# Kernel tuning notes

Hardware: AMD Instinct MI355X
Metric: run time of the kernel (lower is better)

Reference implementation:

```python
import jax, jax.numpy as jnp
import numpy as np

POOL_H, POOL_W = 7, 7
SCALE = 0.25
SAMPLING = 2  # fixed sampling ratio (static grid)


def _sample_coords(lo, bin_sz, pool, s):
    # lo: [N], bin_sz: [N] -> coords [N, pool*s]
    # point iy within bin: (iy + 0.5) / s of a bin
    offs = (jnp.arange(pool)[:, None] + (jnp.arange(s)[None, :] + 0.5) / s).reshape(-1)  # [pool*s]
    return lo[:, None] + offs[None, :] * bin_sz[:, None]


def roi_align(feat, rois, roibatches):
    B, C, H, W = feat.shape
    N = rois.shape[0]
    x1 = rois[:, 0] * SCALE
    y1 = rois[:, 1] * SCALE
    x2 = rois[:, 2] * SCALE
    y2 = rois[:, 3] * SCALE
    roi_w = jnp.maximum(x2 - x1, 1.0)
    roi_h = jnp.maximum(y2 - y1, 1.0)
    bin_w = roi_w / POOL_W
    bin_h = roi_h / POOL_H

    ys = _sample_coords(y1, bin_h, POOL_H, SAMPLING)  # [N, Gy]
    xs = _sample_coords(x1, bin_w, POOL_W, SAMPLING)  # [N, Gx]
    Gy, Gx = ys.shape[1], xs.shape[1]

    vy = (ys >= -1.0) & (ys <= H)  # out-of-range samples contribute 0
    vx = (xs >= -1.0) & (xs <= W)

    yc = jnp.clip(ys, 0.0, H - 1)
    xc = jnp.clip(xs, 0.0, W - 1)
    y_lo = jnp.clip(jnp.floor(yc).astype(jnp.int32), 0, H - 1)
    x_lo = jnp.clip(jnp.floor(xc).astype(jnp.int32), 0, W - 1)
    y_hi = jnp.minimum(y_lo + 1, H - 1)
    x_hi = jnp.minimum(x_lo + 1, W - 1)
    ly = yc - y_lo  # [N, Gy]
    lx = xc - x_lo  # [N, Gx]
    hy = 1.0 - ly
    hx = 1.0 - lx

    b = roibatches.astype(jnp.int32)[:, None, None]  # [N,1,1]

    def gather(yi, xi):
        # advanced indexing -> [N, Gy, Gx, C]
        return feat[b, :, yi[:, :, None], xi[:, None, :]]

    v_ll = gather(y_lo, x_lo)
    v_lh = gather(y_lo, x_hi)
    v_hl = gather(y_hi, x_lo)
    v_hh = gather(y_hi, x_hi)

    wy_l = (hy * vy)[:, :, None, None]
    wy_h = (ly * vy)[:, :, None, None]
    wx_l = (hx * vx)[:, None, :, None]
    wx_h = (lx * vx)[:, None, :, None]

    vals = (wy_l * wx_l * v_ll + wy_l * wx_h * v_lh
            + wy_h * wx_l * v_hl + wy_h * wx_h * v_hh)  # [N, Gy, Gx, C]

    # average pool over the SAMPLING x SAMPLING points per bin
    vals = vals.reshape(N, POOL_H, SAMPLING, POOL_W, SAMPLING, C)
    out = vals.mean(axis=(2, 4))  # [N, POOL_H, POOL_W, C]
    return jnp.transpose(out, (0, 3, 1, 2))  # [N, C, POOL_H, POOL_W]


def setup_inputs() -> dict:
    key = jax.random.key(0)
    k1, k2, k3, k4 = jax.random.split(key, 4)
    B, C, H, W = 4, 256, 200, 304
    N = 1024
    img_h, img_w = H / SCALE, W / SCALE
    feat = jax.random.normal(k1, (B, C, H, W), dtype=jnp.float32)
    xa = jax.random.uniform(k2, (N, 2), minval=0.0, maxval=img_w)
    ya = jax.random.uniform(k3, (N, 2), minval=0.0, maxval=img_h)
    rois = jnp.stack([xa.min(1), ya.min(1), xa.max(1), ya.max(1)], axis=1).astype(jnp.float32)
    roibatches = jax.random.randint(k4, (N,), 0, B, dtype=jnp.int32)
    return {"feat": feat, "rois": rois, "roibatches": roibatches}


def reference(feat, rois, roibatches):
    return roi_align(feat, rois, roibatches)
```

## Files before the change

kernel.cpp:

```cpp
#include <hip/hip_runtime.h>
#include <hip/hip_bf16.h>


#define POOL 7
constexpr int Bc = 4;
constexpr int Cc = 256;
constexpr int Hc = 200;
constexpr int Wc = 304;
constexpr int HWc = Hc * Wc;
constexpr float SCALEc = 0.25f;

static __device__ __forceinline__ float bf16_lo(unsigned u) {
    u <<= 16;
    return __builtin_bit_cast(float, u);
}
static __device__ __forceinline__ float bf16_hi(unsigned u) {
    u &= 0xFFFF0000u;
    return __builtin_bit_cast(float, u);
}
static __device__ __forceinline__ unsigned pack_bf16(float f0, float f1) {
    unsigned u0 = (unsigned)__hip_bfloat16_raw(__float2bfloat16(f0)).x;
    unsigned u1 = (unsigned)__hip_bfloat16_raw(__float2bfloat16(f1)).x;
    return u0 | (u1 << 16);
}

__global__ __launch_bounds__(256) void nchw_to_nhwc_bf16(
    const float* __restrict__ in, ushort* __restrict__ outp)
{
    __shared__ float tile[128][65];
    int b  = blockIdx.z;
    int p0 = blockIdx.x * 64;
    int c0 = blockIdx.y * 128;
    int tx = threadIdx.x;
    int ty = threadIdx.y;

    const float* src = in + ((size_t)b * Cc + c0) * (size_t)HWc + p0;
#pragma unroll
    for (int k = 0; k < 32; ++k) {
        int c = ty + 4 * k;
        tile[c][tx ^ ((c >> 5) & 3)] = src[(size_t)c * HWc + tx];
    }
    __syncthreads();

    int t  = ty * 64 + tx;
    int cg = t & 15;
    int pi = t >> 4;
#pragma unroll
    for (int k = 0; k < 4; ++k) {
        int p = pi + 16 * k;
        unsigned u[4];
#pragma unroll
        for (int j = 0; j < 4; ++j) {
            int ce = cg * 8 + 2 * j;
            int co = ce + 1;
            float f0 = tile[ce][p ^ ((ce >> 5) & 3)];
            float f1 = tile[co][p ^ ((co >> 5) & 3)];
            u[j] = pack_bf16(f0, f1);
        }
        size_t d = ((size_t)b * HWc + p0 + p) * (size_t)Cc + c0 + cg * 8;
        *(uint4*)(outp + d) = make_uint4(u[0], u[1], u[2], u[3]);
    }
}

__global__ __launch_bounds__(512) void roialign_gather(
    const ushort* __restrict__ f,
    const float*  __restrict__ rois,
    const int*    __restrict__ rb,
    float*        __restrict__ out)
{
    __shared__ float stage[49 * 257];

    int n    = blockIdx.x;
    int t    = threadIdx.x;
    int wav  = t >> 6;
    int lane = t & 63;
    int half = lane >> 5;
    int sub  = lane & 31;

    float x1 = rois[n * 4 + 0] * SCALEc;
    float y1 = rois[n * 4 + 1] * SCALEc;
    float x2 = rois[n * 4 + 2] * SCALEc;
    float y2 = rois[n * 4 + 3] * SCALEc;
    int   b  = rb[n];

    float roi_w = fmaxf(x2 - x1, 1.0f);
    float roi_h = fmaxf(y2 - y1, 1.0f);
    float bin_w = roi_w * (1.0f / POOL);
    float bin_h = roi_h * (1.0f / POOL);

    const ushort* base = f + (size_t)b * ((size_t)HWc * Cc) + (size_t)sub * 8;

#pragma unroll 1
    for (int it = 0; it < 4; ++it) {
        int bin = it * 16 + wav * 2 + half;
        if (bin < 49) {
            int ph = bin / POOL;
            int pw = bin % POOL;

            int   yy[2][2];  float wy[2][2];
#pragma unroll
            for (int iy = 0; iy < 2; ++iy) {
                float y  = y1 + ((float)ph + ((float)iy + 0.5f) * 0.5f) * bin_h;
                bool  vy = (y >= -1.0f) && (y <= (float)Hc);
                float yc = fminf(fmaxf(y, 0.0f), (float)(Hc - 1));
                int   y_lo = (int)floorf(yc);
                int   y_hi = min(y_lo + 1, Hc - 1);
                float ly = yc - (float)y_lo;
                yy[iy][0] = y_lo;  yy[iy][1] = y_hi;
                wy[iy][0] = vy ? (1.0f - ly) : 0.0f;
                wy[iy][1] = vy ? ly : 0.0f;
            }
            int   xx[2][2];  float wx[2][2];
#pragma unroll
            for (int ix = 0; ix < 2; ++ix) {
                float x  = x1 + ((float)pw + ((float)ix + 0.5f) * 0.5f) * bin_w;
                bool  vx = (x >= -1.0f) && (x <= (float)Wc);
                float xc = fminf(fmaxf(x, 0.0f), (float)(Wc - 1));
                int   x_lo = (int)floorf(xc);
                int   x_hi = min(x_lo + 1, Wc - 1);
                float lx = xc - (float)x_lo;
                xx[ix][0] = x_lo;  xx[ix][1] = x_hi;
                wx[ix][0] = vx ? (1.0f - lx) : 0.0f;
                wx[ix][1] = vx ? lx : 0.0f;
            }

            float acc[8] = {0.f, 0.f, 0.f, 0.f, 0.f, 0.f, 0.f, 0.f};
#pragma unroll
            for (int iy = 0; iy < 2; ++iy) {
                uint4 v[2][4];
#pragma unroll
                for (int yl = 0; yl < 2; ++yl) {
                    const ushort* row = base + (size_t)yy[iy][yl] * ((size_t)Wc * Cc);
#pragma unroll
                    for (int q = 0; q < 4; ++q) {
                        int ix = q >> 1, xl = q & 1;
                        v[yl][q] = *(const uint4*)(row + (size_t)xx[ix][xl] * Cc);
                    }
                }
#pragma unroll
                for (int yl = 0; yl < 2; ++yl) {
#pragma unroll
                    for (int q = 0; q < 4; ++q) {
                        int ix = q >> 1, xl = q & 1;
                        float w = wy[iy][yl] * wx[ix][xl];
                        const uint4 vv = v[yl][q];
                        acc[0] = fmaf(w, bf16_lo(vv.x), acc[0]);
                        acc[1] = fmaf(w, bf16_hi(vv.x), acc[1]);
                        acc[2] = fmaf(w, bf16_lo(vv.y), acc[2]);
                        acc[3] = fmaf(w, bf16_hi(vv.y), acc[3]);
                        acc[4] = fmaf(w, bf16_lo(vv.z), acc[4]);
                        acc[5] = fmaf(w, bf16_hi(vv.z), acc[5]);
                        acc[6] = fmaf(w, bf16_lo(vv.w), acc[6]);
                        acc[7] = fmaf(w, bf16_hi(vv.w), acc[7]);
                    }
                }
            }
            float* sp = &stage[bin * 257 + sub * 8];
#pragma unroll
            for (int j = 0; j < 8; ++j) sp[j] = acc[j] * 0.25f;
        }
    }
    __syncthreads();

    float* obase = out + (size_t)n * (Cc * POOL * POOL);
#pragma unroll 1
    for (int k = 0; k < 25; ++k) {
        int flat = t + 512 * k;
        if (flat < Cc * POOL * POOL) {
            int c   = flat / 49;
            int bin = flat - c * 49;
            obase[flat] = stage[bin * 257 + c];
        }
    }
}

__global__ __launch_bounds__(256) void roialign_fwd(
    const float* __restrict__ feat,
    const float* __restrict__ rois,
    const int* __restrict__ roibatches,
    float* __restrict__ out,
    int total)
{
    int tid = blockIdx.x * blockDim.x + threadIdx.x;
    if (tid >= total) return;
    int n   = tid / (Cc * POOL * POOL);
    int rem = tid % (Cc * POOL * POOL);
    int c   = rem / (POOL * POOL);
    int bin = rem % (POOL * POOL);
    int ph  = bin / POOL;
    int pw  = bin % POOL;

    float x1 = rois[n * 4 + 0] * SCALEc;
    float y1 = rois[n * 4 + 1] * SCALEc;
    float x2 = rois[n * 4 + 2] * SCALEc;
    float y2 = rois[n * 4 + 3] * SCALEc;
    int   b  = roibatches[n];

    float roi_w = fmaxf(x2 - x1, 1.0f);
    float roi_h = fmaxf(y2 - y1, 1.0f);
    float bin_w = roi_w * (1.0f / POOL);
    float bin_h = roi_h * (1.0f / POOL);

    const float* fp = feat + (size_t)(b * Cc + c) * (size_t)HWc;

    float acc = 0.0f;
#pragma unroll
    for (int iy = 0; iy < 2; ++iy) {
        float y  = y1 + ((float)ph + ((float)iy + 0.5f) * 0.5f) * bin_h;
        bool  vy = (y >= -1.0f) && (y <= (float)Hc);
        float yc = fminf(fmaxf(y, 0.0f), (float)(Hc - 1));
        int   y_lo = (int)floorf(yc);
        int   y_hi = min(y_lo + 1, Hc - 1);
        float ly = yc - (float)y_lo;
        float hy = 1.0f - ly;
        float wyl = vy ? hy : 0.0f;
        float wyh = vy ? ly : 0.0f;
        const float* row_lo = fp + (size_t)y_lo * Wc;
        const float* row_hi = fp + (size_t)y_hi * Wc;
#pragma unroll
        for (int ix = 0; ix < 2; ++ix) {
            float x  = x1 + ((float)pw + ((float)ix + 0.5f) * 0.5f) * bin_w;
            bool  vx = (x >= -1.0f) && (x <= (float)Wc);
            float xc = fminf(fmaxf(x, 0.0f), (float)(Wc - 1));
            int   x_lo = (int)floorf(xc);
            int   x_hi = min(x_lo + 1, Wc - 1);
            float lx = xc - (float)x_lo;
            float hx = 1.0f - lx;
            float wxl = vx ? hx : 0.0f;
            float wxh = vx ? lx : 0.0f;
            acc += wyl * (wxl * row_lo[x_lo] + wxh * row_lo[x_hi])
                 + wyh * (wxl * row_hi[x_lo] + wxh * row_hi[x_hi]);
        }
    }
    out[tid] = acc * 0.25f;
}

extern "C" void kernel_launch(void* const* d_in, const int* in_sizes, int n_in,
                              void* d_out, int out_size, void* d_ws, size_t ws_size,
                              hipStream_t stream)
{
    const float* feat       = (const float*)d_in[0];
    const float* rois       = (const float*)d_in[1];
    const int*   roibatches = (const int*)d_in[2];
    float*       out        = (float*)d_out;
    int N = in_sizes[1] / 4;

    size_t need = (size_t)Bc * HWc * Cc * sizeof(ushort);
    if (ws_size >= need) {
        ushort* fbh = (ushort*)d_ws;
        dim3 tgrid(HWc / 64, Cc / 128, Bc);
        dim3 tblock(64, 4);
        nchw_to_nhwc_bf16<<<tgrid, tblock, 0, stream>>>(feat, fbh);

        roialign_gather<<<N, 512, 0, stream>>>(fbh, rois, roibatches, out);
    } else {
        int total = out_size;
        roialign_fwd<<<(total + 255) / 256, 256, 0, stream>>>(
            feat, rois, roibatches, out, total);
    }
}
```

Measured before the change: 124.1 us.

## Stage RoIAlign bins as packed bf16 in LDS with one bin per wave

```diff
diff --git a/kernel.cpp b/kernel.cpp
--- a/kernel.cpp
+++ b/kernel.cpp
@@ -9,6 +9,7 @@
 constexpr int Wc = 304;
 constexpr int HWc = Hc * Wc;
 constexpr float SCALEc = 0.25f;
+constexpr int STR = 129;
 
 static __device__ __forceinline__ float bf16_lo(unsigned u) {
     u <<= 16;
@@ -62,20 +63,18 @@
     }
 }
 
-__global__ __launch_bounds__(512) void roialign_gather(
+__global__ __launch_bounds__(512, 8) void roialign_gather(
     const ushort* __restrict__ f,
     const float*  __restrict__ rois,
     const int*    __restrict__ rb,
     float*        __restrict__ out)
 {
-    __shared__ float stage[49 * 257];
+    __shared__ unsigned stage[49 * STR];
 
     int n    = blockIdx.x;
     int t    = threadIdx.x;
     int wav  = t >> 6;
     int lane = t & 63;
-    int half = lane >> 5;
-    int sub  = lane & 31;
 
     float x1 = rois[n * 4 + 0] * SCALEc;
     float y1 = rois[n * 4 + 1] * SCALEc;
@@ -88,16 +87,16 @@
     float bin_w = roi_w * (1.0f / POOL);
     float bin_h = roi_h * (1.0f / POOL);
 
-    const ushort* base = f + (size_t)b * ((size_t)HWc * Cc) + (size_t)sub * 8;
+    const uint2* fb = (const uint2*)(f + (size_t)b * ((size_t)HWc * Cc));
 
 #pragma unroll 1
-    for (int it = 0; it < 4; ++it) {
-        int bin = it * 16 + wav * 2 + half;
+    for (int it = 0; it < 7; ++it) {
+        int bin = it * 8 + wav;
         if (bin < 49) {
-            int ph = bin / POOL;
-            int pw = bin % POOL;
-
-            int   yy[2][2];  float wy[2][2];
+            int ph = (bin * 9363) >> 16;
+            int pw = bin - ph * 7;
+
+            unsigned yrow[2][2];  float wy[2][2];
 #pragma unroll
             for (int iy = 0; iy < 2; ++iy) {
                 float y  = y1 + ((float)ph + ((float)iy + 0.5f) * 0.5f) * bin_h;
@@ -106,11 +105,12 @@
                 int   y_lo = (int)floorf(yc);
                 int   y_hi = min(y_lo + 1, Hc - 1);
                 float ly = yc - (float)y_lo;
-                yy[iy][0] = y_lo;  yy[iy][1] = y_hi;
+                yrow[iy][0] = (unsigned)(y_lo * Wc);
+                yrow[iy][1] = (unsigned)(y_hi * Wc);
                 wy[iy][0] = vy ? (1.0f - ly) : 0.0f;
                 wy[iy][1] = vy ? ly : 0.0f;
             }
-            int   xx[2][2];  float wx[2][2];
+            unsigned xo[2][2];  float wx[2][2];
 #pragma unroll
             for (int ix = 0; ix < 2; ++ix) {
                 float x  = x1 + ((float)pw + ((float)ix + 0.5f) * 0.5f) * bin_w;
@@ -119,45 +119,35 @@
                 int   x_lo = (int)floorf(xc);
                 int   x_hi = min(x_lo + 1, Wc - 1);
                 float lx = xc - (float)x_lo;
-                xx[ix][0] = x_lo;  xx[ix][1] = x_hi;
+                xo[ix][0] = (unsigned)x_lo;
+                xo[ix][1] = (unsigned)x_hi;
                 wx[ix][0] = vx ? (1.0f - lx) : 0.0f;
                 wx[ix][1] = vx ? lx : 0.0f;
             }
 
-            float acc[8] = {0.f, 0.f, 0.f, 0.f, 0.f, 0.f, 0.f, 0.f};
+            float acc0 = 0.f, acc1 = 0.f, acc2 = 0.f, acc3 = 0.f;
 #pragma unroll
             for (int iy = 0; iy < 2; ++iy) {
-                uint4 v[2][4];
-#pragma unroll
-                for (int yl = 0; yl < 2; ++yl) {
-                    const ushort* row = base + (size_t)yy[iy][yl] * ((size_t)Wc * Cc);
-#pragma unroll
-                    for (int q = 0; q < 4; ++q) {
-                        int ix = q >> 1, xl = q & 1;
-                        v[yl][q] = *(const uint4*)(row + (size_t)xx[ix][xl] * Cc);
-                    }
+                uint2 v[8];
+#pragma unroll
+                for (int q = 0; q < 8; ++q) {
+                    int yl = q >> 2, ix = (q >> 1) & 1, xl = q & 1;
+                    unsigned p = yrow[iy][yl] + xo[ix][xl];
+                    v[q] = fb[(size_t)(p * 64u + (unsigned)lane)];
                 }
 #pragma unroll
-                for (int yl = 0; yl < 2; ++yl) {
-#pragma unroll
-                    for (int q = 0; q < 4; ++q) {
-                        int ix = q >> 1, xl = q & 1;
-                        float w = wy[iy][yl] * wx[ix][xl];
-                        const uint4 vv = v[yl][q];
-                        acc[0] = fmaf(w, bf16_lo(vv.x), acc[0]);
-                        acc[1] = fmaf(w, bf16_hi(vv.x), acc[1]);
-                        acc[2] = fmaf(w, bf16_lo(vv.y), acc[2]);
-                        acc[3] = fmaf(w, bf16_hi(vv.y), acc[3]);
-                        acc[4] = fmaf(w, bf16_lo(vv.z), acc[4]);
-                        acc[5] = fmaf(w, bf16_hi(vv.z), acc[5]);
-                        acc[6] = fmaf(w, bf16_lo(vv.w), acc[6]);
-                        acc[7] = fmaf(w, bf16_hi(vv.w), acc[7]);
-                    }
+                for (int q = 0; q < 8; ++q) {
+                    int yl = q >> 2, ix = (q >> 1) & 1, xl = q & 1;
+                    float w = wy[iy][yl] * wx[ix][xl];
+                    acc0 = fmaf(w, bf16_lo(v[q].x), acc0);
+                    acc1 = fmaf(w, bf16_hi(v[q].x), acc1);
+                    acc2 = fmaf(w, bf16_lo(v[q].y), acc2);
+                    acc3 = fmaf(w, bf16_hi(v[q].y), acc3);
                 }
             }
-            float* sp = &stage[bin * 257 + sub * 8];
-#pragma unroll
-            for (int j = 0; j < 8; ++j) sp[j] = acc[j] * 0.25f;
+            unsigned w0 = pack_bf16(acc0 * 0.25f, acc1 * 0.25f);
+            unsigned w1 = pack_bf16(acc2 * 0.25f, acc3 * 0.25f);
+            *(uint2*)&stage[bin * STR + lane * 2] = make_uint2(w0, w1);
         }
     }
     __syncthreads();
@@ -167,9 +157,10 @@
     for (int k = 0; k < 25; ++k) {
         int flat = t + 512 * k;
         if (flat < Cc * POOL * POOL) {
-            int c   = flat / 49;
-            int bin = flat - c * 49;
-            obase[flat] = stage[bin * 257 + c];
+            unsigned c   = ((unsigned)flat * 42800u) >> 21;
+            unsigned bin = (unsigned)flat - c * 49u;
+            unsigned u   = stage[bin * STR + (c >> 1)];
+            obase[flat]  = (c & 1) ? bf16_hi(u) : bf16_lo(u);
         }
     }
 }
```

Measured after the change: 126.2 us. About the same (+1.7%).
